# Kernel tuning notes

Measured on AMD Instinct MI355X. Metric: run time of the kernel, lower is better.

## Reference

```python
import jax, jax.numpy as jnp
import numpy as np

H, C = 4, 64            # heads, hidden_channels (per-head dim, concat=False)
N_SRC = N_TGT = 50000
E = 400000
E_LBL = 200000
NEG_SLOPE = 0.2
LN_EPS = 1e-5


def _gatv2(x_src, x_dst, ei, Wl, bl, Wr, br, att, bias, n_dst):
    # PyG GATv2Conv, bipartite, add_self_loops=False, concat=False (mean over heads)
    xl = (x_src @ Wl.T + bl).reshape(x_src.shape[0], H, C)   # lin_l(x_src)
    xr = (x_dst @ Wr.T + br).reshape(x_dst.shape[0], H, C)   # lin_r(x_dst)
    s, d = ei[0], ei[1]
    e = jax.nn.leaky_relu(xl[s] + xr[d], NEG_SLOPE)          # [E,H,C]
    logits = jnp.einsum('ehc,hc->eh', e, att)                # [E,H]
    m = jax.ops.segment_max(logits, d, num_segments=n_dst)
    m = jnp.where(jnp.isfinite(m), m, 0.0)                   # empty segments -> 0
    ex = jnp.exp(logits - m[d])
    den = jax.ops.segment_sum(ex, d, num_segments=n_dst)
    alpha = ex / (den[d] + 1e-16)                            # segment softmax over dst
    out = jax.ops.segment_sum(xl[s] * alpha[:, :, None], d, num_segments=n_dst)
    return out.mean(axis=1) + bias                           # [n_dst, C]


def _layer_norm(x, w, b):
    mu = x.mean(-1, keepdims=True)
    v = ((x - mu) ** 2).mean(-1, keepdims=True)
    return (x - mu) / jnp.sqrt(v + LN_EPS) * w + b


def setup_inputs() -> dict:
    key = jax.random.key(0)
    ks = iter(jax.random.split(key, 64))
    def p(shape, scale=0.1):
        return jax.random.normal(next(ks), shape, jnp.float32) * scale
    inp = {}
    inp['src_emb'] = p((N_SRC, C))
    inp['tgt_emb'] = p((N_TGT, C))
    for name in ['c1st', 'c1ts', 'c2st', 'c2ts']:
        inp[name + '_Wl'] = p((H * C, C))
        inp[name + '_bl'] = jnp.zeros((H * C,), jnp.float32)
        inp[name + '_Wr'] = p((H * C, C))
        inp[name + '_br'] = jnp.zeros((H * C,), jnp.float32)
        inp[name + '_att'] = p((H, C))
        inp[name + '_bias'] = jnp.zeros((C,), jnp.float32)
    inp['ln_s_w'] = jnp.ones((C,), jnp.float32)
    inp['ln_s_b'] = jnp.zeros((C,), jnp.float32)
    inp['ln_t_w'] = jnp.ones((C,), jnp.float32)
    inp['ln_t_b'] = jnp.zeros((C,), jnp.float32)
    inp['node_id_source'] = jnp.arange(N_SRC)
    inp['node_id_target'] = jnp.arange(N_TGT)
    inp['edge_index_st'] = jax.random.randint(next(ks), (2, E), 0, N_SRC)
    inp['edge_index_ts'] = jax.random.randint(next(ks), (2, E), 0, N_TGT)
    inp['edge_label_index'] = jax.random.randint(next(ks), (2, E_LBL), 0, N_SRC)
    return inp


def reference(src_emb, tgt_emb,
              c1st_Wl, c1st_bl, c1st_Wr, c1st_br, c1st_att, c1st_bias,
              c1ts_Wl, c1ts_bl, c1ts_Wr, c1ts_br, c1ts_att, c1ts_bias,
              c2st_Wl, c2st_bl, c2st_Wr, c2st_br, c2st_att, c2st_bias,
              c2ts_Wl, c2ts_bl, c2ts_Wr, c2ts_br, c2ts_att, c2ts_bias,
              ln_s_w, ln_s_b, ln_t_w, ln_t_b,
              node_id_source, node_id_target,
              edge_index_st, edge_index_ts, edge_label_index):
    x_s = src_emb[node_id_source]
    x_t = tgt_emb[node_id_target]
    # layer 1 (to_hetero: one conv per edge type, sum-aggregate per node type)
    h_t = _gatv2(x_s, x_t, edge_index_st, c1st_Wl, c1st_bl, c1st_Wr, c1st_br, c1st_att, c1st_bias, N_TGT)
    h_s = _gatv2(x_t, x_s, edge_index_ts, c1ts_Wl, c1ts_bl, c1ts_Wr, c1ts_br, c1ts_att, c1ts_bias, N_SRC)
    h_s = _layer_norm(jax.nn.relu(h_s), ln_s_w, ln_s_b)
    h_t = _layer_norm(jax.nn.relu(h_t), ln_t_w, ln_t_b)
    # layer 2
    o_t = _gatv2(h_s, h_t, edge_index_st, c2st_Wl, c2st_bl, c2st_Wr, c2st_br, c2st_att, c2st_bias, N_TGT)
    o_s = _gatv2(h_t, h_s, edge_index_ts, c2ts_Wl, c2ts_bl, c2ts_Wr, c2ts_br, c2ts_att, c2ts_bias, N_SRC)
    # classifier: edge-wise dot product
    pred = (o_s[edge_label_index[0]] * o_t[edge_label_index[1]]).sum(axis=-1)
    return pred
```

## Files before the change

kernel.cpp:

```cpp
#include <hip/hip_runtime.h>

#define NEG_SLOPE 0.2f
#define LN_EPS 1e-5f
#define LOG2E 1.44269504088896f

typedef __attribute__((ext_vector_type(8))) short bf16x8;
typedef __attribute__((ext_vector_type(4))) float f32x4;
typedef __attribute__((ext_vector_type(2))) float f32x2;

__device__ __forceinline__ short f2bf(float f) {
    unsigned u = __float_as_uint(f);
    return (short)((u + 0x7FFFu + ((u >> 16) & 1u)) >> 16);
}

#define DPP_ADD(v, ctrl) \
    v += __int_as_float(__builtin_amdgcn_update_dpp(0, __float_as_int(v), ctrl, 0xF, 0xF, true))
__device__ __forceinline__ float dpp_sum16(float v) {
    DPP_ADD(v, 0xB1);
    DPP_ADD(v, 0x4E);
    DPP_ADD(v, 0x141);
    DPP_ADD(v, 0x140);
    return v;
}

__device__ __forceinline__ void unpack4(uint2 w, f32x2& lo, f32x2& hi) {
    lo.x = __uint_as_float(w.x << 16);
    lo.y = __uint_as_float(w.x & 0xFFFF0000u);
    hi.x = __uint_as_float(w.y << 16);
    hi.y = __uint_as_float(w.y & 0xFFFF0000u);
}

struct LinJob {
    const float* x; const int* ids; const float* W; const float* bias;
    unsigned short* out; int n;
};
struct LinJob4 { LinJob j[4]; };

__global__ __launch_bounds__(256) void lin4_kernel(LinJob4 P, int bpj)
{
    int jid = blockIdx.x / bpj;
    LinJob job = P.j[jid];
    int blk = blockIdx.x - jid * bpj;
    const float* __restrict__ x = job.x;
    const int* __restrict__ ids = job.ids;
    const float* __restrict__ W = job.W;
    int n = job.n;

    int wv = threadIdx.x >> 6;
    int lane = threadIdx.x & 63;
    int m = lane & 15, q = lane >> 4;
    bf16x8 wfrag[4][2];
#pragma unroll
    for (int t = 0; t < 4; ++t) {
        int ncol = wv * 64 + t * 16 + m;
        const float* wr = W + ncol * 64 + q * 8;
#pragma unroll
        for (int h = 0; h < 2; ++h) {
            const float4* p = (const float4*)(wr + h * 32);
            float4 u = p[0], v = p[1];
            bf16x8 f;
            f[0]=f2bf(u.x); f[1]=f2bf(u.y); f[2]=f2bf(u.z); f[3]=f2bf(u.w);
            f[4]=f2bf(v.x); f[5]=f2bf(v.y); f[6]=f2bf(v.z); f[7]=f2bf(v.w);
            wfrag[t][h] = f;
        }
    }
    float4 biasv[4];
#pragma unroll
    for (int t = 0; t < 4; ++t)
        biasv[t] = *(const float4*)(job.bias + wv * 64 + t * 16 + q * 4);

    int ntiles = (n + 15) >> 4;
    for (int tile = blk; tile < ntiles; tile += bpj) {
        int row = tile * 16 + m;
        int rc = row < n ? row : n - 1;
        int src = ids ? ids[rc] : rc;
        const float* xr = x + (size_t)src * 64 + q * 8;
        bf16x8 xfrag[2];
#pragma unroll
        for (int h = 0; h < 2; ++h) {
            const float4* p = (const float4*)(xr + h * 32);
            float4 u = p[0], v = p[1];
            bf16x8 f;
            f[0]=f2bf(u.x); f[1]=f2bf(u.y); f[2]=f2bf(u.z); f[3]=f2bf(u.w);
            f[4]=f2bf(v.x); f[5]=f2bf(v.y); f[6]=f2bf(v.z); f[7]=f2bf(v.w);
            xfrag[h] = f;
        }
        bool valid = row < n;
        unsigned short* orow = job.out + (size_t)row * 256 + wv * 64 + q * 4;
#pragma unroll
        for (int t = 0; t < 4; ++t) {
            f32x4 acc = {0.f, 0.f, 0.f, 0.f};
            acc = __builtin_amdgcn_mfma_f32_16x16x32_bf16(wfrag[t][0], xfrag[0], acc, 0, 0, 0);
            acc = __builtin_amdgcn_mfma_f32_16x16x32_bf16(wfrag[t][1], xfrag[1], acc, 0, 0, 0);
            if (valid) {
                ushort4 o;
                o.x = (unsigned short)f2bf(acc[0] + biasv[t].x);
                o.y = (unsigned short)f2bf(acc[1] + biasv[t].y);
                o.z = (unsigned short)f2bf(acc[2] + biasv[t].z);
                o.w = (unsigned short)f2bf(acc[3] + biasv[t].w);
                *(ushort4*)(orow + t * 16) = o;
            }
        }
    }
}

__global__ __launch_bounds__(256) void hist2_kernel(
    const int* __restrict__ ed0, int E0, int* __restrict__ cnt0,
    const int* __restrict__ ed1, int E1, int* __restrict__ cnt1)
{
    int i = blockIdx.x * 256 + threadIdx.x;
    if (i < E0) atomicAdd(&cnt0[ed0[i]], 1);
    else { int k = i - E0; if (k < E1) atomicAdd(&cnt1[ed1[k]], 1); }
}

__global__ __launch_bounds__(256) void chunk_sum2_kernel(
    const int* __restrict__ cnt0, int* __restrict__ csum0, int n0, int nc0,
    const int* __restrict__ cnt1, int* __restrict__ csum1, int n1)
{
    const int* cnt; int* csum; int n; int blk;
    if (blockIdx.x < (unsigned)nc0) { cnt = cnt0; csum = csum0; n = n0; blk = blockIdx.x; }
    else { cnt = cnt1; csum = csum1; n = n1; blk = blockIdx.x - nc0; }
    __shared__ int wsm[4];
    int tid = threadIdx.x;
    int base = blk * 1024 + tid * 4;
    int s = 0;
#pragma unroll
    for (int k = 0; k < 4; ++k) { int i = base + k; if (i < n) s += cnt[i]; }
#pragma unroll
    for (int ofs = 32; ofs > 0; ofs >>= 1) s += __shfl_xor(s, ofs, 64);
    if ((tid & 63) == 0) wsm[tid >> 6] = s;
    __syncthreads();
    if (tid == 0) csum[blk] = wsm[0] + wsm[1] + wsm[2] + wsm[3];
}

__global__ __launch_bounds__(128) void chunk_scan2_kernel(
    int* __restrict__ c0, int n0, int* __restrict__ c1, int n1)
{
    int w = threadIdx.x >> 6, lane = threadIdx.x & 63;
    int* c = w ? c1 : c0;
    int n = w ? n1 : n0;
    int v = (lane < n) ? c[lane] : 0;
    int incl = v;
#pragma unroll
    for (int ofs = 1; ofs < 64; ofs <<= 1) {
        int t = __shfl_up(incl, ofs, 64);
        if (lane >= ofs) incl += t;
    }
    if (lane < n) c[lane] = incl - v;
}

__global__ __launch_bounds__(1024) void scan_apply2_kernel(
    const int* __restrict__ cnt0, const int* __restrict__ co0, int* __restrict__ offs0, int n0, int nc0,
    const int* __restrict__ cnt1, const int* __restrict__ co1, int* __restrict__ offs1, int n1)
{
    const int* cnt; const int* co; int* offs; int n; int blk;
    if (blockIdx.x < (unsigned)nc0) { cnt = cnt0; co = co0; offs = offs0; n = n0; blk = blockIdx.x; }
    else { cnt = cnt1; co = co1; offs = offs1; n = n1; blk = blockIdx.x - nc0; }
    __shared__ int wsum[16];
    int tid = threadIdx.x, lane = tid & 63, w = tid >> 6;
    int i = blk * 1024 + tid;
    int v = (i < n) ? cnt[i] : 0;
    int incl = v;
#pragma unroll
    for (int ofs = 1; ofs < 64; ofs <<= 1) {
        int t = __shfl_up(incl, ofs, 64);
        if (lane >= ofs) incl += t;
    }
    if (lane == 63) wsum[w] = incl;
    __syncthreads();
    if (w == 0) {
        int x = (lane < 16) ? wsum[lane] : 0;
#pragma unroll
        for (int ofs = 1; ofs < 16; ofs <<= 1) {
            int t = __shfl_up(x, ofs, 64);
            if (lane >= ofs) x += t;
        }
        if (lane < 16) wsum[lane] = x;
    }
    __syncthreads();
    int woff = (w == 0) ? 0 : wsum[w - 1];
    if (i < n) offs[i + 1] = co[blk] + woff + incl;
    if (i == 0) offs[0] = 0;
}

__global__ __launch_bounds__(256) void fill2_kernel(
    const int* __restrict__ es0, const int* __restrict__ ed0,
    const int* __restrict__ offs0, int* __restrict__ cur0, int* __restrict__ srt0, int E0,
    const int* __restrict__ es1, const int* __restrict__ ed1,
    const int* __restrict__ offs1, int* __restrict__ cur1, int* __restrict__ srt1, int E1)
{
    int i = blockIdx.x * 256 + threadIdx.x;
    if (i < E0) {
        int d = ed0[i];
        int pos = offs0[d] + atomicAdd(&cur0[d], 1);
        srt0[pos] = es0[i];
    } else {
        int k = i - E0;
        if (k < E1) {
            int d = ed1[k];
            int pos = offs1[d] + atomicAdd(&cur1[d], 1);
            srt1[pos] = es1[k];
        }
    }
}

struct GatJob {
    const unsigned short* A; const unsigned short* B;
    const int* offs; const int* srt;
    const float* att; const float* bias;
    const float* lnw; const float* lnb;
    float* out; int n_dst;
};

__global__ __launch_bounds__(256) void gat2_kernel(GatJob j0, GatJob j1, int blocks0)
{
    GatJob job = (blockIdx.x < (unsigned)blocks0) ? j0 : j1;
    int blk = (blockIdx.x < (unsigned)blocks0) ? blockIdx.x : blockIdx.x - blocks0;
    int d = blk * 4 + (threadIdx.x >> 6);
    int lane = threadIdx.x & 63;
    if (d >= job.n_dst) return;
    int g = lane & 15;
    const uint2* __restrict__ A2 = (const uint2*)job.A;
    float4 att4 = ((const float4*)job.att)[lane];
    f32x2 att01 = {att4.x * LOG2E, att4.y * LOG2E};
    f32x2 att23 = {att4.z * LOG2E, att4.w * LOG2E};
    uint2 bw = ((const uint2*)(job.B + (size_t)d * 256))[lane];
    f32x2 b01, b23; unpack4(bw, b01, b23);
    const f32x2 z2 = {0.f, 0.f};

    float den1 = 0.f, den2 = 0.f;
    f32x2 p01 = z2, p23 = z2, q01 = z2, q23 = z2;
    const int* __restrict__ srt = job.srt;
    int j0i = __builtin_amdgcn_readfirstlane(job.offs[d]);
    int j1i = __builtin_amdgcn_readfirstlane(job.offs[d + 1]);
    int j = j0i;

#define EDGE(S, DEN, A01, A23) { \
        const uint2* rowp = A2 + (size_t)(S) * 64;    \
        uint2 wbits = rowp[lane];                     \
        f32x2 a01, a23; unpack4(wbits, a01, a23); \
        f32x2 t01 = a01 + b01, t23 = a23 + b23; \
        f32x2 l01 = __builtin_elementwise_max(t01 * NEG_SLOPE, t01); \
        f32x2 l23 = __builtin_elementwise_max(t23 * NEG_SLOPE, t23); \
        f32x2 dp = l01 * att01 + l23 * att23; \
        float p = dpp_sum16(dp.x + dp.y); \
        float pe = __builtin_amdgcn_exp2f(p); \
        DEN += pe; \
        A01 = a01 * pe + A01; \
        A23 = a23 * pe + A23; }

    for (; j + 1 < j1i; j += 2) {
        int s0 = __builtin_amdgcn_readfirstlane(srt[j]);
        int s1 = __builtin_amdgcn_readfirstlane(srt[j + 1]);
        EDGE(s0, den1, p01, p23)
        EDGE(s1, den2, q01, q23)
    }
    if (j < j1i) {
        int s0 = __builtin_amdgcn_readfirstlane(srt[j]);
        EDGE(s0, den1, p01, p23)
    }
#undef EDGE

    float den = den1 + den2;
    f32x2 A01 = p01 + q01, A23 = p23 + q23;
    float inv = 1.f / (den + 1e-16f);
    A01 *= inv; A23 *= inv;
    float4 acc = {A01.x, A01.y, A23.x, A23.y};
    acc.x += __shfl_xor(acc.x, 16, 64);
    acc.y += __shfl_xor(acc.y, 16, 64);
    acc.z += __shfl_xor(acc.z, 16, 64);
    acc.w += __shfl_xor(acc.w, 16, 64);
    acc.x += __shfl_xor(acc.x, 32, 64);
    acc.y += __shfl_xor(acc.y, 32, 64);
    acc.z += __shfl_xor(acc.z, 32, 64);
    acc.w += __shfl_xor(acc.w, 32, 64);
    float4 b4 = ((const float4*)job.bias)[g];
    float4 v;
    v.x = acc.x * 0.25f + b4.x;
    v.y = acc.y * 0.25f + b4.y;
    v.z = acc.z * 0.25f + b4.z;
    v.w = acc.w * 0.25f + b4.w;
    if (job.lnw) {
        v.x = v.x > 0.f ? v.x : 0.f;
        v.y = v.y > 0.f ? v.y : 0.f;
        v.z = v.z > 0.f ? v.z : 0.f;
        v.w = v.w > 0.f ? v.w : 0.f;
        float s  = dpp_sum16(v.x + v.y + v.z + v.w);
        float ss = dpp_sum16(v.x*v.x + v.y*v.y + v.z*v.z + v.w*v.w);
        float mu = s * (1.f / 64.f);
        float var = ss * (1.f / 64.f) - mu * mu;
        float rs = rsqrtf(var + LN_EPS);
        float4 w4 = ((const float4*)job.lnw)[g];
        float4 l4 = ((const float4*)job.lnb)[g];
        v.x = (v.x - mu) * rs * w4.x + l4.x;
        v.y = (v.y - mu) * rs * w4.y + l4.y;
        v.z = (v.z - mu) * rs * w4.z + l4.z;
        v.w = (v.w - mu) * rs * w4.w + l4.w;
    }
    if (lane < 16) ((float4*)(job.out + (size_t)d * 64))[g] = v;
}

__global__ __launch_bounds__(256) void dot_kernel(
    const float* __restrict__ os, const float* __restrict__ ot,
    const int* __restrict__ ea, const int* __restrict__ eb,
    float* __restrict__ out, int n)
{
    int e = (int)((blockIdx.x * 256u + threadIdx.x) >> 4);
    int l = threadIdx.x & 15;
    if (e >= n) return;
    float4 a = ((const float4*)(os + (size_t)ea[e] * 64))[l];
    float4 b = ((const float4*)(ot + (size_t)eb[e] * 64))[l];
    float v = dpp_sum16(a.x * b.x + a.y * b.y + a.z * b.z + a.w * b.w);
    if (l == 0) out[e] = v;
}

extern "C" void kernel_launch(void* const* d_in, const int* in_sizes, int n_in,
                              void* d_out, int out_size, void* d_ws, size_t ws_size,
                              hipStream_t stream)
{
    const float* src_emb = (const float*)d_in[0];
    const float* tgt_emb = (const float*)d_in[1];
    const float* P[4][6];
    for (int ci = 0; ci < 4; ++ci)
        for (int k = 0; k < 6; ++k)
            P[ci][k] = (const float*)d_in[2 + ci * 6 + k];
    const float* ln_s_w = (const float*)d_in[26];
    const float* ln_s_b = (const float*)d_in[27];
    const float* ln_t_w = (const float*)d_in[28];
    const float* ln_t_b = (const float*)d_in[29];
    const int* nid_s = (const int*)d_in[30];
    const int* nid_t = (const int*)d_in[31];
    const int* ei_st = (const int*)d_in[32];
    const int* ei_ts = (const int*)d_in[33];
    const int* eli   = (const int*)d_in[34];

    int n_src = in_sizes[30];
    int n_tgt = in_sizes[31];
    int E_st = in_sizes[32] / 2;
    int E_ts = in_sizes[33] / 2;
    int EL   = in_sizes[34] / 2;
    int nmax = n_src > n_tgt ? n_src : n_tgt;

    float* ws = (float*)d_ws;
    size_t off = 0;
    auto alloc = [&](size_t count) {
        float* p = ws + off;
        off += (count + 63) & ~(size_t)63;
        return p;
    };
    unsigned short* A_st = (unsigned short*)alloc((size_t)nmax * 128);
    unsigned short* B_st = (unsigned short*)alloc((size_t)nmax * 128);
    unsigned short* A_ts = (unsigned short*)alloc((size_t)nmax * 128);
    unsigned short* B_ts = (unsigned short*)alloc((size_t)nmax * 128);
    int*   offs_st = (int*)alloc((size_t)n_tgt + 1);
    int*   srt_st  = (int*)alloc((size_t)E_st);
    int*   offs_ts = (int*)alloc((size_t)n_src + 1);
    int*   srt_ts  = (int*)alloc((size_t)E_ts);
    int*   zeros   = (int*)alloc((size_t)4 * nmax);
    int*   csum0   = (int*)alloc(64);
    int*   csum1   = (int*)alloc(64);
    float* h_s     = alloc((size_t)n_src * 64);
    float* h_t     = alloc((size_t)n_tgt * 64);
    float* o_s     = alloc((size_t)n_src * 64);
    float* o_t     = alloc((size_t)n_tgt * 64);
    if (off * sizeof(float) > ws_size) return;

    int* cnt0 = zeros;
    int* cnt1 = zeros + nmax;
    int* cur0 = zeros + 2 * (size_t)nmax;
    int* cur1 = zeros + 3 * (size_t)nmax;

    int nc0 = (n_tgt + 1023) / 1024, nc1 = (n_src + 1023) / 1024;
    hipMemsetAsync(zeros, 0, (size_t)4 * nmax * sizeof(int), stream);
    hist2_kernel<<<(E_st + E_ts + 255) / 256, 256, 0, stream>>>(
        ei_st + E_st, E_st, cnt0, ei_ts + E_ts, E_ts, cnt1);
    chunk_sum2_kernel<<<nc0 + nc1, 256, 0, stream>>>(cnt0, csum0, n_tgt, nc0, cnt1, csum1, n_src);
    chunk_scan2_kernel<<<1, 128, 0, stream>>>(csum0, nc0, csum1, nc1);
    scan_apply2_kernel<<<nc0 + nc1, 1024, 0, stream>>>(
        cnt0, csum0, offs_st, n_tgt, nc0, cnt1, csum1, offs_ts, n_src);
    fill2_kernel<<<(E_st + E_ts + 255) / 256, 256, 0, stream>>>(
        ei_st, ei_st + E_st, offs_st, cur0, srt_st, E_st,
        ei_ts, ei_ts + E_ts, offs_ts, cur1, srt_ts, E_ts);

    int bpj = (nmax + 63) / 64;

    auto lin_layer = [&](const float* xs, const int* ids_s, int ns,
                         const float* xt, const int* ids_t, int nt,
                         const float* const* pst, const float* const* pts) {
        LinJob4 LJ;
        LJ.j[0] = { xs, ids_s, pst[0], pst[1], A_st, ns };
        LJ.j[1] = { xt, ids_t, pst[2], pst[3], B_st, nt };
        LJ.j[2] = { xt, ids_t, pts[0], pts[1], A_ts, nt };
        LJ.j[3] = { xs, ids_s, pts[2], pts[3], B_ts, ns };
        lin4_kernel<<<4 * bpj, 256, 0, stream>>>(LJ, bpj);
    };
    auto gat_layer = [&](const float* const* pst, const float* const* pts,
                         const float* lnw_t, const float* lnb_t,
                         const float* lnw_s, const float* lnb_s,
                         float* out_t, float* out_s) {
        GatJob g0 = { A_st, B_st, offs_st, srt_st, pst[4], pst[5], lnw_t, lnb_t, out_t, n_tgt };
        GatJob g1 = { A_ts, B_ts, offs_ts, srt_ts, pts[4], pts[5], lnw_s, lnb_s, out_s, n_src };
        int b0 = (n_tgt + 3) / 4, b1 = (n_src + 3) / 4;
        gat2_kernel<<<b0 + b1, 256, 0, stream>>>(g0, g1, b0);
    };

    lin_layer(src_emb, nid_s, n_src, tgt_emb, nid_t, n_tgt, P[0], P[1]);
    gat_layer(P[0], P[1], ln_t_w, ln_t_b, ln_s_w, ln_s_b, h_t, h_s);

    lin_layer(h_s, nullptr, n_src, h_t, nullptr, n_tgt, P[2], P[3]);
    gat_layer(P[2], P[3], nullptr, nullptr, nullptr, nullptr, o_t, o_s);

    dot_kernel<<<((size_t)EL * 16 + 255) / 256, 256, 0, stream>>>(
        o_s, o_t, eli, eli + EL, (float*)d_out, EL);
}
```

Baseline: 491.3 us.

## Store intermediate node features in bf16 and pre-convert weights once

Layer outputs h_s/h_t/o_s/o_t are now written as bf16 instead of fp32, halving the bytes read by the second linear layer and the dot-product classifier. Weight matrices are converted to bf16 once by a small prep kernel instead of every lin block converting them per launch. The lin grid is fixed to 256 blocks per job, so each block loops over more tiles. This adds an extra launch and rounds intermediate activations to bf16, which loses some precision.

```diff
diff --git a/kernel.cpp b/kernel.cpp
--- a/kernel.cpp
+++ b/kernel.cpp
@@ -30,9 +30,24 @@
     hi.y = __uint_as_float(w.y & 0xFFFF0000u);
 }
 
+struct WSrc8 { const float* s[8]; };
+__global__ __launch_bounds__(256) void wprep_kernel(WSrc8 W, unsigned short* dst)
+{
+    int gidx = blockIdx.x * 256 + threadIdx.x;
+    int mid = gidx >> 12;
+    int within = (gidx & 4095) * 4;
+    float4 v = *(const float4*)(W.s[mid] + within);
+    ushort4 o;
+    o.x = (unsigned short)f2bf(v.x);
+    o.y = (unsigned short)f2bf(v.y);
+    o.z = (unsigned short)f2bf(v.z);
+    o.w = (unsigned short)f2bf(v.w);
+    *(ushort4*)(dst + mid * 16384 + within) = o;
+}
+
 struct LinJob {
-    const float* x; const int* ids; const float* W; const float* bias;
-    unsigned short* out; int n;
+    const void* x; const int* ids; const unsigned short* Wb; const float* bias;
+    unsigned short* out; int n; int xbf16;
 };
 struct LinJob4 { LinJob j[4]; };
 
@@ -41,9 +56,7 @@
     int jid = blockIdx.x / bpj;
     LinJob job = P.j[jid];
     int blk = blockIdx.x - jid * bpj;
-    const float* __restrict__ x = job.x;
     const int* __restrict__ ids = job.ids;
-    const float* __restrict__ W = job.W;
     int n = job.n;
 
     int wv = threadIdx.x >> 6;
@@ -53,16 +66,10 @@
 #pragma unroll
     for (int t = 0; t < 4; ++t) {
         int ncol = wv * 64 + t * 16 + m;
-        const float* wr = W + ncol * 64 + q * 8;
-#pragma unroll
-        for (int h = 0; h < 2; ++h) {
-            const float4* p = (const float4*)(wr + h * 32);
-            float4 u = p[0], v = p[1];
-            bf16x8 f;
-            f[0]=f2bf(u.x); f[1]=f2bf(u.y); f[2]=f2bf(u.z); f[3]=f2bf(u.w);
-            f[4]=f2bf(v.x); f[5]=f2bf(v.y); f[6]=f2bf(v.z); f[7]=f2bf(v.w);
-            wfrag[t][h] = f;
-        }
+        const unsigned short* wr = job.Wb + ncol * 64 + q * 8;
+#pragma unroll
+        for (int h = 0; h < 2; ++h)
+            wfrag[t][h] = *(const bf16x8*)(wr + h * 32);
     }
     float4 biasv[4];
 #pragma unroll
@@ -74,16 +81,23 @@
         int row = tile * 16 + m;
         int rc = row < n ? row : n - 1;
         int src = ids ? ids[rc] : rc;
-        const float* xr = x + (size_t)src * 64 + q * 8;
         bf16x8 xfrag[2];
-#pragma unroll
-        for (int h = 0; h < 2; ++h) {
-            const float4* p = (const float4*)(xr + h * 32);
-            float4 u = p[0], v = p[1];
-            bf16x8 f;
-            f[0]=f2bf(u.x); f[1]=f2bf(u.y); f[2]=f2bf(u.z); f[3]=f2bf(u.w);
-            f[4]=f2bf(v.x); f[5]=f2bf(v.y); f[6]=f2bf(v.z); f[7]=f2bf(v.w);
-            xfrag[h] = f;
+        if (job.xbf16) {
+            const unsigned short* xr = (const unsigned short*)job.x + (size_t)src * 64 + q * 8;
+#pragma unroll
+            for (int h = 0; h < 2; ++h)
+                xfrag[h] = *(const bf16x8*)(xr + h * 32);
+        } else {
+            const float* xr = (const float*)job.x + (size_t)src * 64 + q * 8;
+#pragma unroll
+            for (int h = 0; h < 2; ++h) {
+                const float4* p = (const float4*)(xr + h * 32);
+                float4 u = p[0], v = p[1];
+                bf16x8 f;
+                f[0]=f2bf(u.x); f[1]=f2bf(u.y); f[2]=f2bf(u.z); f[3]=f2bf(u.w);
+                f[4]=f2bf(v.x); f[5]=f2bf(v.y); f[6]=f2bf(v.z); f[7]=f2bf(v.w);
+                xfrag[h] = f;
+            }
         }
         bool valid = row < n;
         unsigned short* orow = job.out + (size_t)row * 256 + wv * 64 + q * 4;
@@ -209,7 +223,7 @@
     const int* offs; const int* srt;
     const float* att; const float* bias;
     const float* lnw; const float* lnb;
-    float* out; int n_dst;
+    unsigned short* out; int n_dst;
 };
 
 __global__ __launch_bounds__(256) void gat2_kernel(GatJob j0, GatJob j1, int blocks0)
@@ -297,20 +311,31 @@
         v.z = (v.z - mu) * rs * w4.z + l4.z;
         v.w = (v.w - mu) * rs * w4.w + l4.w;
     }
-    if (lane < 16) ((float4*)(job.out + (size_t)d * 64))[g] = v;
+    if (lane < 16) {
+        ushort4 o;
+        o.x = (unsigned short)f2bf(v.x);
+        o.y = (unsigned short)f2bf(v.y);
+        o.z = (unsigned short)f2bf(v.z);
+        o.w = (unsigned short)f2bf(v.w);
+        *(ushort4*)(job.out + (size_t)d * 64 + g * 4) = o;
+    }
 }
 
 __global__ __launch_bounds__(256) void dot_kernel(
-    const float* __restrict__ os, const float* __restrict__ ot,
+    const unsigned short* __restrict__ os, const unsigned short* __restrict__ ot,
     const int* __restrict__ ea, const int* __restrict__ eb,
     float* __restrict__ out, int n)
 {
     int e = (int)((blockIdx.x * 256u + threadIdx.x) >> 4);
     int l = threadIdx.x & 15;
     if (e >= n) return;
-    float4 a = ((const float4*)(os + (size_t)ea[e] * 64))[l];
-    float4 b = ((const float4*)(ot + (size_t)eb[e] * 64))[l];
-    float v = dpp_sum16(a.x * b.x + a.y * b.y + a.z * b.z + a.w * b.w);
+    uint2 aw = ((const uint2*)(os + (size_t)ea[e] * 64))[l];
+    uint2 bw = ((const uint2*)(ot + (size_t)eb[e] * 64))[l];
+    f32x2 a01, a23, b01, b23;
+    unpack4(aw, a01, a23);
+    unpack4(bw, b01, b23);
+    f32x2 dp = a01 * b01 + a23 * b23;
+    float v = dpp_sum16(dp.x + dp.y);
     if (l == 0) out[e] = v;
 }
 
@@ -352,6 +377,7 @@
     unsigned short* B_st = (unsigned short*)alloc((size_t)nmax * 128);
     unsigned short* A_ts = (unsigned short*)alloc((size_t)nmax * 128);
     unsigned short* B_ts = (unsigned short*)alloc((size_t)nmax * 128);
+    unsigned short* Wbf  = (unsigned short*)alloc(65536);
     int*   offs_st = (int*)alloc((size_t)n_tgt + 1);
     int*   srt_st  = (int*)alloc((size_t)E_st);
     int*   offs_ts = (int*)alloc((size_t)n_src + 1);
@@ -359,16 +385,20 @@
     int*   zeros   = (int*)alloc((size_t)4 * nmax);
     int*   csum0   = (int*)alloc(64);
     int*   csum1   = (int*)alloc(64);
-    float* h_s     = alloc((size_t)n_src * 64);
-    float* h_t     = alloc((size_t)n_tgt * 64);
-    float* o_s     = alloc((size_t)n_src * 64);
-    float* o_t     = alloc((size_t)n_tgt * 64);
+    unsigned short* h_s = (unsigned short*)alloc((size_t)n_src * 32);
+    unsigned short* h_t = (unsigned short*)alloc((size_t)n_tgt * 32);
+    unsigned short* o_s = (unsigned short*)alloc((size_t)n_src * 32);
+    unsigned short* o_t = (unsigned short*)alloc((size_t)n_tgt * 32);
     if (off * sizeof(float) > ws_size) return;
 
     int* cnt0 = zeros;
     int* cnt1 = zeros + nmax;
     int* cur0 = zeros + 2 * (size_t)nmax;
     int* cur1 = zeros + 3 * (size_t)nmax;
+
+    WSrc8 WS;
+    for (int ci = 0; ci < 4; ++ci) { WS.s[ci*2] = P[ci][0]; WS.s[ci*2+1] = P[ci][2]; }
+    wprep_kernel<<<128, 256, 0, stream>>>(WS, Wbf);
 
     int nc0 = (n_tgt + 1023) / 1024, nc1 = (n_src + 1023) / 1024;
     hipMemsetAsync(zeros, 0, (size_t)4 * nmax * sizeof(int), stream);
@@ -382,32 +412,33 @@
         ei_st, ei_st + E_st, offs_st, cur0, srt_st, E_st,
         ei_ts, ei_ts + E_ts, offs_ts, cur1, srt_ts, E_ts);
 
-    int bpj = (nmax + 63) / 64;
-
-    auto lin_layer = [&](const float* xs, const int* ids_s, int ns,
-                         const float* xt, const int* ids_t, int nt,
+    int bpj = 256;
+
+    auto lin_layer = [&](const void* xs, const int* ids_s, int ns,
+                         const void* xt, const int* ids_t, int nt, int xbf,
+                         int slot_base,
                          const float* const* pst, const float* const* pts) {
         LinJob4 LJ;
-        LJ.j[0] = { xs, ids_s, pst[0], pst[1], A_st, ns };
-        LJ.j[1] = { xt, ids_t, pst[2], pst[3], B_st, nt };
-        LJ.j[2] = { xt, ids_t, pts[0], pts[1], A_ts, nt };
-        LJ.j[3] = { xs, ids_s, pts[2], pts[3], B_ts, ns };
+        LJ.j[0] = { xs, ids_s, Wbf + (slot_base+0)*16384, pst[1], A_st, ns, xbf };
+        LJ.j[1] = { xt, ids_t, Wbf + (slot_base+1)*16384, pst[3], B_st, nt, xbf };
+        LJ.j[2] = { xt, ids_t, Wbf + (slot_base+2)*16384, pts[1], A_ts, nt, xbf };
+        LJ.j[3] = { xs, ids_s, Wbf + (slot_base+3)*16384, pts[3], B_ts, ns, xbf };
         lin4_kernel<<<4 * bpj, 256, 0, stream>>>(LJ, bpj);
     };
     auto gat_layer = [&](const float* const* pst, const float* const* pts,
                          const float* lnw_t, const float* lnb_t,
                          const float* lnw_s, const float* lnb_s,
-                         float* out_t, float* out_s) {
+                         unsigned short* out_t, unsigned short* out_s) {
         GatJob g0 = { A_st, B_st, offs_st, srt_st, pst[4], pst[5], lnw_t, lnb_t, out_t, n_tgt };
         GatJob g1 = { A_ts, B_ts, offs_ts, srt_ts, pts[4], pts[5], lnw_s, lnb_s, out_s, n_src };
         int b0 = (n_tgt + 3) / 4, b1 = (n_src + 3) / 4;
         gat2_kernel<<<b0 + b1, 256, 0, stream>>>(g0, g1, b0);
     };
 
-    lin_layer(src_emb, nid_s, n_src, tgt_emb, nid_t, n_tgt, P[0], P[1]);
+    lin_layer(src_emb, nid_s, n_src, tgt_emb, nid_t, n_tgt, 0, 0, P[0], P[1]);
     gat_layer(P[0], P[1], ln_t_w, ln_t_b, ln_s_w, ln_s_b, h_t, h_s);
 
-    lin_layer(h_s, nullptr, n_src, h_t, nullptr, n_tgt, P[2], P[3]);
+    lin_layer(h_s, nullptr, n_src, h_t, nullptr, n_tgt, 1, 4, P[2], P[3]);
     gat_layer(P[2], P[3], nullptr, nullptr, nullptr, nullptr, o_t, o_s);
 
     dot_kernel<<<((size_t)EL * 16 + 255) / 256, 256, 0, stream>>>(
```

After: 439.7 us. 1.12x faster.
